# Kernel tuning notes

Measured on AMD Instinct MI355X. Metric: run time of the kernel, lower is better.

The kernel has to match this reference:

```python
import jax, jax.numpy as jnp
import numpy as np

L, B, T, D, H = 2, 64, 1024, 512, 512


def setup_inputs() -> dict:
    key = jax.random.key(0)
    k0, k1, k2 = jax.random.split(key, 3)
    std = 1.0 / np.sqrt(H)
    x = jax.random.normal(k0, (B, T, D), dtype=jnp.float32)
    # fused gate weights, slice order [i, f, o, c] along the 4H axis
    Wx = jax.random.uniform(k1, (L, 4 * H, D), jnp.float32, -std, std)
    Wh = jax.random.uniform(k2, (L, 4 * H, H), jnp.float32, -std, std)
    bx = jnp.zeros((L, 4 * H), jnp.float32)  # Linear biases (input side)
    bh = jnp.zeros((L, 4 * H), jnp.float32)  # Linear biases (hidden side)
    # extra gate biases b_i,b_f,b_o,b_c: b_f initialized to ones
    bext = jnp.zeros((L, 4 * H), jnp.float32).at[:, H:2 * H].set(1.0)
    return {"x": x, "Wx": Wx, "bx": bx, "Wh": Wh, "bh": bh, "bext": bext}


def _run_layer(x_tbd, Wx_l, b_l, Wh_l):
    # precompute all input-side gate pre-activations in one big GEMM: (T,B,4H)
    xg = jnp.einsum('tbd,gd->tbg', x_tbd, Wx_l) + b_l
    h0 = jnp.zeros((B, H), x_tbd.dtype)

    def step(carry, xg_t):
        h, c, n = carry
        g = xg_t + h @ Wh_l.T  # (B,4H)
        i, f, o, u = jnp.split(g, 4, axis=-1)
        i = jax.nn.sigmoid(i)
        f = jax.nn.sigmoid(f)
        o = jax.nn.sigmoid(o)
        u = jnp.tanh(u)
        c = f * c + i * u
        n = jnp.clip(f * n + i, 1e-6, 1e6)
        h = o * jnp.tanh(c / n)
        return (h, c, n), h

    (hN, cN, nN), hs = jax.lax.scan(step, (h0, h0, h0), xg)
    return hs, hN, cN, nN  # hs: (T,B,H)


def reference(x, Wx, bx, Wh, bh, bext):
    layer_in = jnp.transpose(x, (1, 0, 2))  # (T,B,D)
    hNs, cNs, nNs = [], [], []
    for l in range(L):
        b_l = bx[l] + bh[l] + bext[l]
        layer_in, hN, cN, nN = _run_layer(layer_in, Wx[l], b_l, Wh[l])
        hNs.append(hN); cNs.append(cN); nNs.append(nN)
    out = jnp.transpose(layer_in, (1, 0, 2))  # (B,T,H)
    return out, jnp.stack(hNs), jnp.stack(cNs), jnp.stack(nNs)
```

## Files before the change

### kernel.cpp

```cpp
#include <hip/hip_runtime.h>
#include <hip/hip_bf16.h>

#define B_   64
#define T_   1024
#define D_   512
#define H_   512
#define G4H  2048
#define K_   1024

typedef __bf16 bf16x8 __attribute__((ext_vector_type(8)));
typedef float  f32x4  __attribute__((ext_vector_type(4)));

#define OFF_XT  0ull
#define OFF_H1  (OFF_XT + (unsigned long long)T_*B_*D_*2)
#define OFF_H2  (OFF_H1 + (unsigned long long)T_*B_*H_*2)
#define OFF_WP  (OFF_H2 + (unsigned long long)T_*B_*H_*2)
#define OFF_ZB  (OFF_WP + (unsigned long long)2*G4H*K_*2)
#define OFF_FLG (OFF_ZB + 16384ull)
#define OUT_HN  33554432ull

__global__ void prep_kernel(const float* __restrict__ x, const float* __restrict__ Wx,
                            const float* __restrict__ Wh, unsigned char* __restrict__ ws)
{
    unsigned tid = blockIdx.x * 256u + threadIdx.x;
    __hip_bfloat16* xT = (__hip_bfloat16*)(ws + OFF_XT);
    __hip_bfloat16* Wp = (__hip_bfloat16*)(ws + OFF_WP);

    {
        unsigned base = tid * 8u;
        unsigned d  = base & (D_ - 1);
        unsigned bt = base >> 9;
        unsigned t  = bt & (T_ - 1);
        unsigned b  = bt >> 10;
        const float* src = x + base;
        __hip_bfloat16* dst = xT + ((unsigned long long)t * B_ + b) * D_ + d;
        float4 f0 = *(const float4*)(src);
        float4 f1 = *(const float4*)(src + 4);
        dst[0] = __float2bfloat16(f0.x); dst[1] = __float2bfloat16(f0.y);
        dst[2] = __float2bfloat16(f0.z); dst[3] = __float2bfloat16(f0.w);
        dst[4] = __float2bfloat16(f1.x); dst[5] = __float2bfloat16(f1.y);
        dst[6] = __float2bfloat16(f1.z); dst[7] = __float2bfloat16(f1.w);
    }
    {
        unsigned i = tid;
        unsigned k = i & (K_ - 1);
        unsigned r = (i >> 10) & (G4H - 1);
        unsigned l = i >> 21;
        float v = (k < D_) ? Wx[((unsigned long long)l * G4H + r) * D_ + k]
                           : Wh[((unsigned long long)l * G4H + r) * H_ + (k - D_)];
        Wp[i] = __float2bfloat16(v);
    }
    if (tid < 8192u) ((__hip_bfloat16*)(ws + OFF_ZB))[tid] = __float2bfloat16(0.f);
    if (tid < 4096u) ((int*)(ws + OFF_FLG))[tid] = 0;
}

__device__ __forceinline__ unsigned bf16_bits(float f)
{
    union { __hip_bfloat16 h; unsigned short u; } c;
    c.h = __float2bfloat16(f);
    return (unsigned)c.u;
}

__launch_bounds__(64, 1)
__global__ void slstm_persist(const float* __restrict__ bx, const float* __restrict__ bh,
                              const float* __restrict__ bext, unsigned char* ws,
                              float* __restrict__ out)
{
    const int lane = threadIdx.x;
    const int n    = lane & 15;
    const int quad = lane >> 4;
    const int blk  = blockIdx.x;
    const int chain = blk & 7;
    const int w     = blk >> 3;
    const int layer = chain >> 2;
    const int g     = chain & 3;
    const int hid_base   = w * 8;
    const int batch_base = g * 16;

    const __hip_bfloat16* xT = (const __hip_bfloat16*)(ws + OFF_XT);
    __hip_bfloat16* h1buf = (__hip_bfloat16*)(ws + OFF_H1);
    __hip_bfloat16* h2buf = (__hip_bfloat16*)(ws + OFF_H2);
    const __hip_bfloat16* Wp = (const __hip_bfloat16*)(ws + OFF_WP);
    const __hip_bfloat16* zb = (const __hip_bfloat16*)(ws + OFF_ZB);
    int* flags = (int*)(ws + OFF_FLG);
    int* myf = flags + chain * 64;
    int* prf = flags + g * 64;

    const int r0 = (n < 8) ? (hid_base + n) : (2*H_ + hid_base + n - 8);
    const int r1 = (n < 8) ? (H_ + hid_base + n) : (3*H_ + hid_base + n - 8);
    const float bias0 = bx[layer*G4H + r0] + bh[layer*G4H + r0] + bext[layer*G4H + r0];
    const float bias1 = bx[layer*G4H + r1] + bh[layer*G4H + r1] + bext[layer*G4H + r1];

    const __hip_bfloat16* Wl = Wp + (unsigned long long)layer * G4H * K_;
    bf16x8 B0[32], B1[32];
#pragma unroll
    for (int kt = 0; kt < 32; ++kt) {
        B0[kt] = *(const bf16x8*)(Wl + (unsigned long long)r0 * K_ + kt*32 + quad*8);
        B1[kt] = *(const bf16x8*)(Wl + (unsigned long long)r1 * K_ + kt*32 + quad*8);
    }

    const __hip_bfloat16* xin  = (layer == 0) ? xT : h1buf;
    __hip_bfloat16*       hout = (layer == 0) ? h1buf : h2buf;

    float cst[4] = {0.f,0.f,0.f,0.f}, nst[4] = {0.f,0.f,0.f,0.f};

#pragma unroll 1
    for (int t = 0; t < T_; ++t) {
        bf16x8 a[32];
        const __hip_bfloat16* Ax = xin + ((unsigned long long)t * B_ + batch_base + n) * D_ + quad*8;

        if (layer == 0) {
#pragma unroll
            for (int kt = 0; kt < 16; ++kt) a[kt] = *(const bf16x8*)(Ax + kt*32);
            asm volatile("" ::: "memory");
            if (t > 0) {
                for (;;) {
                    int v = __hip_atomic_load(myf + lane, __ATOMIC_RELAXED, __HIP_MEMORY_SCOPE_AGENT);
                    if (__all(v >= t)) break;
                }
            }
        } else {
            for (;;) {
                int v1 = __hip_atomic_load(myf + lane, __ATOMIC_RELAXED, __HIP_MEMORY_SCOPE_AGENT);
                int v2 = __hip_atomic_load(prf + lane, __ATOMIC_RELAXED, __HIP_MEMORY_SCOPE_AGENT);
                if (__all((v1 >= t) & (v2 >= t + 1))) break;
            }
        }
        asm volatile("" ::: "memory");

        if (layer == 1) {
#pragma unroll
            for (int kt = 0; kt < 16; ++kt) a[kt] = *(const bf16x8*)(Ax + kt*32);
        }
        const __hip_bfloat16* Ah = (t == 0)
            ? (zb + n * H_ + quad*8)
            : (hout + ((unsigned long long)(t-1) * B_ + batch_base + n) * H_ + quad*8);
#pragma unroll
        for (int kt = 0; kt < 16; ++kt) a[16+kt] = *(const bf16x8*)(Ah + kt*32);

        f32x4 acc0 = {0.f,0.f,0.f,0.f}, acc1 = {0.f,0.f,0.f,0.f};
#pragma unroll
        for (int kt = 0; kt < 32; ++kt) {
            acc0 = __builtin_amdgcn_mfma_f32_16x16x32_bf16(a[kt], B0[kt], acc0, 0, 0, 0);
            acc1 = __builtin_amdgcn_mfma_f32_16x16x32_bf16(a[kt], B1[kt], acc1, 0, 0, 0);
        }

        float hv[4];
#pragma unroll
        for (int r = 0; r < 4; ++r) {
            float v0 = acc0[r] + bias0;
            float v1 = acc1[r] + bias1;
            float act0 = 1.f / (1.f + __expf(-v0));
            float pre  = (n < 8) ? -v1 : -2.f*v1;
            float s    = 1.f / (1.f + __expf(pre));
            float act1 = (n < 8) ? s : (2.f*s - 1.f);
            float o_ = __shfl_xor(act0, 8);
            float u_ = __shfl_xor(act1, 8);
            float ci = act1 * cst[r] + act0 * u_;
            float ni = fminf(fmaxf(act1 * nst[r] + act0, 1e-6f), 1e6f);
            cst[r] = ci; nst[r] = ni;
            float ratio = ci / ni;
            float e2 = __expf(-2.f * ratio);
            float th = (1.f - e2) / (1.f + e2);
            hv[r] = o_ * th;
        }

#pragma unroll
        for (int r = 0; r < 4; ++r) {
            unsigned mybits = bf16_bits(hv[r]);
            unsigned other  = (unsigned)__shfl_xor((int)mybits, 1);
            if ((n & 1) == 0 && n < 8) {
                const int b = batch_base + quad*4 + r;
                unsigned pack = (mybits & 0xffffu) | (other << 16);
                unsigned* p = (unsigned*)(hout + ((unsigned long long)t * B_ + b) * H_ + hid_base + n);
                __hip_atomic_store(p, pack, __ATOMIC_RELAXED, __HIP_MEMORY_SCOPE_AGENT);
            }
        }

        if (n < 8) {
            const int hid = hid_base + n;
            if (layer == 1) {
#pragma unroll
                for (int r = 0; r < 4; ++r) {
                    const int b = batch_base + quad*4 + r;
                    out[((unsigned long long)b * T_ + t) * H_ + hid] = hv[r];
                }
            }
            if (t == T_ - 1) {
#pragma unroll
                for (int r = 0; r < 4; ++r) {
                    const int b = batch_base + quad*4 + r;
                    unsigned long long so = OUT_HN + (unsigned long long)layer*32768ull
                                          + (unsigned long long)b*H_ + hid;
                    out[so]            = hv[r];
                    out[so +  65536ull] = cst[r];
                    out[so + 131072ull] = nst[r];
                }
            }
        }

        asm volatile("s_waitcnt vmcnt(0)" ::: "memory");
        if (lane == 0)
            __hip_atomic_store(myf + w, t + 1, __ATOMIC_RELAXED, __HIP_MEMORY_SCOPE_AGENT);
    }
}

extern "C" void kernel_launch(void* const* d_in, const int* in_sizes, int n_in,
                              void* d_out, int out_size, void* d_ws, size_t ws_size,
                              hipStream_t stream)
{
    const float* x    = (const float*)d_in[0];
    const float* Wx   = (const float*)d_in[1];
    const float* bx   = (const float*)d_in[2];
    const float* Wh   = (const float*)d_in[3];
    const float* bh   = (const float*)d_in[4];
    const float* bext = (const float*)d_in[5];
    float* out = (float*)d_out;
    unsigned char* ws = (unsigned char*)d_ws;

    prep_kernel<<<16384, 256, 0, stream>>>(x, Wx, Wh, ws);
    slstm_persist<<<512, 64, 0, stream>>>(bx, bh, bext, ws, out);
}
```

Baseline: 6.644 ms.

## Replace per-step flag synchronization with sentinel-based polling on hidden-state data

Drops the per-workgroup progress flags and instead pre-fills the h1/h2 buffers with a NaN sentinel pattern. Consumers poll the actual h fragments they need with system-coherent loads until no sentinel remains, so readiness and data arrive in one load instead of a flag round-trip plus a dependent load. This removes the producer's vmcnt(0) wait and flag store from the critical path of each recurrent step. The cost is more polling traffic over full fragments, plus reliance on the packed 32-bit stores being atomic and on real outputs never matching the sentinel bits.

```diff
diff --git a/kernel.cpp b/kernel.cpp
--- a/kernel.cpp
+++ b/kernel.cpp
@@ -10,13 +10,15 @@
 
 typedef __bf16 bf16x8 __attribute__((ext_vector_type(8)));
 typedef float  f32x4  __attribute__((ext_vector_type(4)));
+typedef int    i32x4  __attribute__((ext_vector_type(4)));
+
+#define SENT 0x7FC07FC0
 
 #define OFF_XT  0ull
 #define OFF_H1  (OFF_XT + (unsigned long long)T_*B_*D_*2)
 #define OFF_H2  (OFF_H1 + (unsigned long long)T_*B_*H_*2)
 #define OFF_WP  (OFF_H2 + (unsigned long long)T_*B_*H_*2)
 #define OFF_ZB  (OFF_WP + (unsigned long long)2*G4H*K_*2)
-#define OFF_FLG (OFF_ZB + 16384ull)
 #define OUT_HN  33554432ull
 
 __global__ void prep_kernel(const float* __restrict__ x, const float* __restrict__ Wx,
@@ -50,8 +52,12 @@
                            : Wh[((unsigned long long)l * G4H + r) * H_ + (k - D_)];
         Wp[i] = __float2bfloat16(v);
     }
+    {
+        uint4 s; s.x = s.y = s.z = s.w = SENT;
+        uint4* p = (uint4*)(ws + OFF_H1) + (unsigned long long)tid * 2u;
+        p[0] = s; p[1] = s;
+    }
     if (tid < 8192u) ((__hip_bfloat16*)(ws + OFF_ZB))[tid] = __float2bfloat16(0.f);
-    if (tid < 4096u) ((int*)(ws + OFF_FLG))[tid] = 0;
 }
 
 __device__ __forceinline__ unsigned bf16_bits(float f)
@@ -59,6 +65,31 @@
     union { __hip_bfloat16 h; unsigned short u; } c;
     c.h = __float2bfloat16(f);
     return (unsigned)c.u;
+}
+
+#define PLD(dst, base, OFFS) \
+    asm volatile("global_load_dwordx4 %0, %1, off offset:" OFFS " sc0 sc1" \
+                 : "=v"(dst) : "v"(base))
+
+#define POLL16(buf, base)                                  \
+    PLD(buf[0],  base, "0");   PLD(buf[1],  base, "64");   \
+    PLD(buf[2],  base, "128"); PLD(buf[3],  base, "192");  \
+    PLD(buf[4],  base, "256"); PLD(buf[5],  base, "320");  \
+    PLD(buf[6],  base, "384"); PLD(buf[7],  base, "448");  \
+    PLD(buf[8],  base, "512"); PLD(buf[9],  base, "576");  \
+    PLD(buf[10], base, "640"); PLD(buf[11], base, "704");  \
+    PLD(buf[12], base, "768"); PLD(buf[13], base, "832");  \
+    PLD(buf[14], base, "896"); PLD(buf[15], base, "960")
+
+template<int CNT>
+__device__ __forceinline__ int frag_ok(const i32x4* v)
+{
+    int ok = 1;
+#pragma unroll
+    for (int i = 0; i < CNT; ++i)
+        ok &= (v[i][0] != (int)SENT) & (v[i][1] != (int)SENT) &
+              (v[i][2] != (int)SENT) & (v[i][3] != (int)SENT);
+    return ok;
 }
 
 __launch_bounds__(64, 1)
@@ -82,9 +113,6 @@
     __hip_bfloat16* h2buf = (__hip_bfloat16*)(ws + OFF_H2);
     const __hip_bfloat16* Wp = (const __hip_bfloat16*)(ws + OFF_WP);
     const __hip_bfloat16* zb = (const __hip_bfloat16*)(ws + OFF_ZB);
-    int* flags = (int*)(ws + OFF_FLG);
-    int* myf = flags + chain * 64;
-    int* prf = flags + g * 64;
 
     const int r0 = (n < 8) ? (hid_base + n) : (2*H_ + hid_base + n - 8);
     const int r1 = (n < 8) ? (H_ + hid_base + n) : (3*H_ + hid_base + n - 8);
@@ -108,35 +136,56 @@
     for (int t = 0; t < T_; ++t) {
         bf16x8 a[32];
         const __hip_bfloat16* Ax = xin + ((unsigned long long)t * B_ + batch_base + n) * D_ + quad*8;
+        const __hip_bfloat16* Ah = hout + ((unsigned long long)(t-1) * B_ + batch_base + n) * H_ + quad*8;
 
         if (layer == 0) {
 #pragma unroll
             for (int kt = 0; kt < 16; ++kt) a[kt] = *(const bf16x8*)(Ax + kt*32);
-            asm volatile("" ::: "memory");
-            if (t > 0) {
+            if (t == 0) {
+#pragma unroll
+                for (int kt = 0; kt < 16; ++kt)
+                    a[16+kt] = *(const bf16x8*)(zb + n * H_ + quad*8 + kt*32);
+            } else {
+                i32x4 hb[16];
                 for (;;) {
-                    int v = __hip_atomic_load(myf + lane, __ATOMIC_RELAXED, __HIP_MEMORY_SCOPE_AGENT);
-                    if (__all(v >= t)) break;
-                }
+                    POLL16(hb, Ah);
+                    asm volatile("s_waitcnt vmcnt(0)" ::: "memory");
+                    __builtin_amdgcn_sched_barrier(0);
+                    if (__all(frag_ok<16>(hb))) break;
+                }
+#pragma unroll
+                for (int kt = 0; kt < 16; ++kt) a[16+kt] = __builtin_bit_cast(bf16x8, hb[kt]);
             }
         } else {
-            for (;;) {
-                int v1 = __hip_atomic_load(myf + lane, __ATOMIC_RELAXED, __HIP_MEMORY_SCOPE_AGENT);
-                int v2 = __hip_atomic_load(prf + lane, __ATOMIC_RELAXED, __HIP_MEMORY_SCOPE_AGENT);
-                if (__all((v1 >= t) & (v2 >= t + 1))) break;
-            }
-        }
-        asm volatile("" ::: "memory");
-
-        if (layer == 1) {
-#pragma unroll
-            for (int kt = 0; kt < 16; ++kt) a[kt] = *(const bf16x8*)(Ax + kt*32);
-        }
-        const __hip_bfloat16* Ah = (t == 0)
-            ? (zb + n * H_ + quad*8)
-            : (hout + ((unsigned long long)(t-1) * B_ + batch_base + n) * H_ + quad*8);
-#pragma unroll
-        for (int kt = 0; kt < 16; ++kt) a[16+kt] = *(const bf16x8*)(Ah + kt*32);
+            if (t == 0) {
+                i32x4 xb[16];
+                for (;;) {
+                    POLL16(xb, Ax);
+                    asm volatile("s_waitcnt vmcnt(0)" ::: "memory");
+                    __builtin_amdgcn_sched_barrier(0);
+                    if (__all(frag_ok<16>(xb))) break;
+                }
+#pragma unroll
+                for (int kt = 0; kt < 16; ++kt) a[kt] = __builtin_bit_cast(bf16x8, xb[kt]);
+#pragma unroll
+                for (int kt = 0; kt < 16; ++kt)
+                    a[16+kt] = *(const bf16x8*)(zb + n * H_ + quad*8 + kt*32);
+            } else {
+                i32x4 xb[16], hb[16];
+                for (;;) {
+                    POLL16(xb, Ax);
+                    POLL16(hb, Ah);
+                    asm volatile("s_waitcnt vmcnt(0)" ::: "memory");
+                    __builtin_amdgcn_sched_barrier(0);
+                    int ok = frag_ok<16>(xb) & frag_ok<16>(hb);
+                    if (__all(ok)) break;
+                }
+#pragma unroll
+                for (int kt = 0; kt < 16; ++kt) a[kt]    = __builtin_bit_cast(bf16x8, xb[kt]);
+#pragma unroll
+                for (int kt = 0; kt < 16; ++kt) a[16+kt] = __builtin_bit_cast(bf16x8, hb[kt]);
+            }
+        }
 
         f32x4 acc0 = {0.f,0.f,0.f,0.f}, acc1 = {0.f,0.f,0.f,0.f};
 #pragma unroll
@@ -163,10 +212,7 @@
             float e2 = __expf(-2.f * ratio);
             float th = (1.f - e2) / (1.f + e2);
             hv[r] = o_ * th;
-        }
-
-#pragma unroll
-        for (int r = 0; r < 4; ++r) {
+
             unsigned mybits = bf16_bits(hv[r]);
             unsigned other  = (unsigned)__shfl_xor((int)mybits, 1);
             if ((n & 1) == 0 && n < 8) {
@@ -198,10 +244,6 @@
                 }
             }
         }
-
-        asm volatile("s_waitcnt vmcnt(0)" ::: "memory");
-        if (lane == 0)
-            __hip_atomic_store(myf + w, t + 1, __ATOMIC_RELAXED, __HIP_MEMORY_SCOPE_AGENT);
     }
 }
 
```

Result: slower. 8.093 ms (+21.8%).

## Group four waves per workgroup to cut inter-block flag polling, prefetch next x

Applied to the files above, without the earlier changes.

Launches 128 workgroups of 256 threads instead of 512 single-wave blocks. Each workgroup covers 32 hidden units and publishes one flag after a __syncthreads, so each chain polls 16 flags rather than 64. Layer 0 now loads the next timestep's input slice ahead of the flag wait, and s_sleep is added to the spin loops. The cost is a block-wide barrier every step, and a wave that lags delays the whole workgroup's flag.

```diff
diff --git a/kernel.cpp b/kernel.cpp
--- a/kernel.cpp
+++ b/kernel.cpp
@@ -61,20 +61,22 @@
     return (unsigned)c.u;
 }
 
-__launch_bounds__(64, 1)
+__launch_bounds__(256, 1)
 __global__ void slstm_persist(const float* __restrict__ bx, const float* __restrict__ bh,
                               const float* __restrict__ bext, unsigned char* ws,
                               float* __restrict__ out)
 {
-    const int lane = threadIdx.x;
+    const int tid  = threadIdx.x;
+    const int lane = tid & 63;
+    const int wv   = tid >> 6;
     const int n    = lane & 15;
     const int quad = lane >> 4;
     const int blk  = blockIdx.x;
     const int chain = blk & 7;
-    const int w     = blk >> 3;
+    const int w2    = blk >> 3;
     const int layer = chain >> 2;
     const int g     = chain & 3;
-    const int hid_base   = w * 8;
+    const int hid_base   = w2 * 32 + wv * 8;
     const int batch_base = g * 16;
 
     const __hip_bfloat16* xT = (const __hip_bfloat16*)(ws + OFF_XT);
@@ -83,8 +85,8 @@
     const __hip_bfloat16* Wp = (const __hip_bfloat16*)(ws + OFF_WP);
     const __hip_bfloat16* zb = (const __hip_bfloat16*)(ws + OFF_ZB);
     int* flags = (int*)(ws + OFF_FLG);
-    int* myf = flags + chain * 64;
-    int* prf = flags + g * 64;
+    int* myf = flags + chain * 16;
+    int* prf = flags + g * 16;
 
     const int r0 = (n < 8) ? (hid_base + n) : (2*H_ + hid_base + n - 8);
     const int r1 = (n < 8) ? (H_ + hid_base + n) : (3*H_ + hid_base + n - 8);
@@ -104,45 +106,57 @@
 
     float cst[4] = {0.f,0.f,0.f,0.f}, nst[4] = {0.f,0.f,0.f,0.f};
 
+    bf16x8 axv[16];
+    if (layer == 0) {
+        const __hip_bfloat16* Ax0 = xin + ((unsigned long long)(batch_base + n)) * D_ + quad*8;
+#pragma unroll
+        for (int kt = 0; kt < 16; ++kt) axv[kt] = *(const bf16x8*)(Ax0 + kt*32);
+    }
+
 #pragma unroll 1
     for (int t = 0; t < T_; ++t) {
-        bf16x8 a[32];
-        const __hip_bfloat16* Ax = xin + ((unsigned long long)t * B_ + batch_base + n) * D_ + quad*8;
-
-        if (layer == 0) {
-#pragma unroll
-            for (int kt = 0; kt < 16; ++kt) a[kt] = *(const bf16x8*)(Ax + kt*32);
-            asm volatile("" ::: "memory");
-            if (t > 0) {
-                for (;;) {
-                    int v = __hip_atomic_load(myf + lane, __ATOMIC_RELAXED, __HIP_MEMORY_SCOPE_AGENT);
-                    if (__all(v >= t)) break;
+        if (layer == 1) {
+            for (;;) {
+                int v2 = __hip_atomic_load(prf + (lane & 15), __ATOMIC_RELAXED, __HIP_MEMORY_SCOPE_AGENT);
+                int ok = (v2 >= t + 1);
+                if (t > 0) {
+                    int v1 = __hip_atomic_load(myf + (lane & 15), __ATOMIC_RELAXED, __HIP_MEMORY_SCOPE_AGENT);
+                    ok &= (v1 >= t);
                 }
-            }
-        } else {
+                if (__all(ok)) break;
+                __builtin_amdgcn_s_sleep(1);
+            }
+        } else if (t > 0) {
             for (;;) {
-                int v1 = __hip_atomic_load(myf + lane, __ATOMIC_RELAXED, __HIP_MEMORY_SCOPE_AGENT);
-                int v2 = __hip_atomic_load(prf + lane, __ATOMIC_RELAXED, __HIP_MEMORY_SCOPE_AGENT);
-                if (__all((v1 >= t) & (v2 >= t + 1))) break;
+                int v = __hip_atomic_load(myf + (lane & 15), __ATOMIC_RELAXED, __HIP_MEMORY_SCOPE_AGENT);
+                if (__all(v >= t)) break;
+                __builtin_amdgcn_s_sleep(1);
             }
         }
         asm volatile("" ::: "memory");
 
         if (layer == 1) {
-#pragma unroll
-            for (int kt = 0; kt < 16; ++kt) a[kt] = *(const bf16x8*)(Ax + kt*32);
+            const __hip_bfloat16* Ax = xin + ((unsigned long long)t * B_ + batch_base + n) * D_ + quad*8;
+#pragma unroll
+            for (int kt = 0; kt < 16; ++kt) axv[kt] = *(const bf16x8*)(Ax + kt*32);
         }
         const __hip_bfloat16* Ah = (t == 0)
             ? (zb + n * H_ + quad*8)
             : (hout + ((unsigned long long)(t-1) * B_ + batch_base + n) * H_ + quad*8);
-#pragma unroll
-        for (int kt = 0; kt < 16; ++kt) a[16+kt] = *(const bf16x8*)(Ah + kt*32);
+        bf16x8 ah[16];
+#pragma unroll
+        for (int kt = 0; kt < 16; ++kt) ah[kt] = *(const bf16x8*)(Ah + kt*32);
 
         f32x4 acc0 = {0.f,0.f,0.f,0.f}, acc1 = {0.f,0.f,0.f,0.f};
 #pragma unroll
-        for (int kt = 0; kt < 32; ++kt) {
-            acc0 = __builtin_amdgcn_mfma_f32_16x16x32_bf16(a[kt], B0[kt], acc0, 0, 0, 0);
-            acc1 = __builtin_amdgcn_mfma_f32_16x16x32_bf16(a[kt], B1[kt], acc1, 0, 0, 0);
+        for (int kt = 0; kt < 16; ++kt) {
+            acc0 = __builtin_amdgcn_mfma_f32_16x16x32_bf16(axv[kt], B0[kt], acc0, 0, 0, 0);
+            acc1 = __builtin_amdgcn_mfma_f32_16x16x32_bf16(axv[kt], B1[kt], acc1, 0, 0, 0);
+        }
+#pragma unroll
+        for (int kt = 0; kt < 16; ++kt) {
+            acc0 = __builtin_amdgcn_mfma_f32_16x16x32_bf16(ah[kt], B0[16+kt], acc0, 0, 0, 0);
+            acc1 = __builtin_amdgcn_mfma_f32_16x16x32_bf16(ah[kt], B1[16+kt], acc1, 0, 0, 0);
         }
 
         float hv[4];
@@ -163,10 +177,7 @@
             float e2 = __expf(-2.f * ratio);
             float th = (1.f - e2) / (1.f + e2);
             hv[r] = o_ * th;
-        }
-
-#pragma unroll
-        for (int r = 0; r < 4; ++r) {
+
             unsigned mybits = bf16_bits(hv[r]);
             unsigned other  = (unsigned)__shfl_xor((int)mybits, 1);
             if ((n & 1) == 0 && n < 8) {
@@ -199,9 +210,16 @@
             }
         }
 
+        if (layer == 0 && t + 1 < T_) {
+            const __hip_bfloat16* Axn = xin + ((unsigned long long)(t+1) * B_ + batch_base + n) * D_ + quad*8;
+#pragma unroll
+            for (int kt = 0; kt < 16; ++kt) axv[kt] = *(const bf16x8*)(Axn + kt*32);
+        }
+
         asm volatile("s_waitcnt vmcnt(0)" ::: "memory");
-        if (lane == 0)
-            __hip_atomic_store(myf + w, t + 1, __ATOMIC_RELAXED, __HIP_MEMORY_SCOPE_AGENT);
+        __syncthreads();
+        if (tid == 0)
+            __hip_atomic_store(myf + w2, t + 1, __ATOMIC_RELAXED, __HIP_MEMORY_SCOPE_AGENT);
     }
 }
 
@@ -219,5 +237,5 @@
     unsigned char* ws = (unsigned char*)d_ws;
 
     prep_kernel<<<16384, 256, 0, stream>>>(x, Wx, Wh, ws);
-    slstm_persist<<<512, 64, 0, stream>>>(bx, bh, bext, ws, out);
-}
+    slstm_persist<<<128, 256, 0, stream>>>(bx, bh, bext, ws, out);
+}
```

Measured after the change: 7.864 ms. 18.4% more time.
